# Kernel optimization log

Measured on AMD Instinct MI355X. Metric: run time of the kernel, lower is better.

The kernel has to match this reference:

```python
import jax, jax.numpy as jnp
import numpy as np
from jax import lax

EPS = 1e-5

@jax.custom_vjp
def bin_active(x):
    # forward: sign binarization (original also returns channel-mean of |x|, which is discarded)
    return jnp.sign(x)

def _ba_fwd(x):
    return jnp.sign(x), x

def _ba_bwd(x, g):
    # straight-through estimator: zero grad where |x| >= 1
    return (jnp.where((x >= 1.0) | (x <= -1.0), 0.0, g),)

bin_active.defvjp(_ba_fwd, _ba_bwd)


def setup_inputs() -> dict:
    key = jax.random.key(0)
    k1, k2 = jax.random.split(key)
    N, C_in, H, W_sp = 64, 256, 56, 56
    C_out, K = 256, 3
    x = jax.random.normal(k1, (N, C_in, H, W_sp), dtype=jnp.float32)
    gamma = jnp.ones((C_in,), dtype=jnp.float32)
    beta = jnp.zeros((C_in,), dtype=jnp.float32)
    W = jax.random.normal(k2, (C_out, C_in, K, K), dtype=jnp.float32) * 0.05
    return {"x": x, "gamma": gamma, "beta": beta, "W": W}


def reference(x, gamma, beta, W):
    # BatchNorm2d (training-mode batch stats), affine
    mean = jnp.mean(x, axis=(0, 2, 3), keepdims=True)          # [1,C,1,1]
    var = jnp.var(x, axis=(0, 2, 3), keepdims=True)
    xn = (x - mean) * lax.rsqrt(var + EPS)
    xn = xn * gamma.reshape(1, -1, 1, 1) + beta.reshape(1, -1, 1, 1)
    # binarize activations
    xb = bin_active(xn)
    # Conv2d stride=1 pad=1, no bias, then ReLU
    y = lax.conv_general_dilated(
        xb, W,
        window_strides=(1, 1),
        padding=[(1, 1), (1, 1)],
        dimension_numbers=("NCHW", "OIHW", "NCHW"),
    )
    return jax.nn.relu(y)
```

## Files before the change

kernel.cpp:

```cpp
#include <hip/hip_runtime.h>
#include <hip/hip_bf16.h>
#include <stdint.h>

#define HP 58
#define CIN 256
#define COUT 256
#define HH 56
#define WW 56
#define XROW 14848
#define IMG_STRIDE (HP*XROW)
#define NPIX 200704.0

#define XO    16
#define SROW  928
#define AO    89600
#define LDS_TOTAL 155136

typedef __attribute__((ext_vector_type(4)))  int i32x4;
typedef __attribute__((ext_vector_type(16))) int i32x16;

#define GLDS(g, l) __builtin_amdgcn_global_load_lds( \
    (const __attribute__((address_space(1))) void*)(g), \
    (__attribute__((address_space(3))) void*)(l), 16, 0, 0)

__global__ __launch_bounds__(256) void stats_partial(const float* __restrict__ x,
                                                     double* __restrict__ part) {
  int b = blockIdx.x;
  int c = b >> 6, n = b & 63;
  const float4* p = (const float4*)(x + (size_t)(n*CIN + c) * (HH*WW));
  double s = 0.0, s2 = 0.0;
  for (int i = threadIdx.x; i < 784; i += 256) {
    float4 v = p[i];
    double a0 = v.x, a1 = v.y, a2 = v.z, a3 = v.w;
    s  += (a0 + a1) + (a2 + a3);
    s2 += (a0*a0 + a1*a1) + (a2*a2 + a3*a3);
  }
  for (int off = 32; off > 0; off >>= 1) {
    s  += __shfl_down(s, off);
    s2 += __shfl_down(s2, off);
  }
  __shared__ double red[8];
  int wv = threadIdx.x >> 6, ln = threadIdx.x & 63;
  if (ln == 0) { red[wv*2] = s; red[wv*2+1] = s2; }
  __syncthreads();
  if (threadIdx.x == 0) {
    double ts = ((red[0]+red[2])+red[4])+red[6];
    double t2 = ((red[1]+red[3])+red[5])+red[7];
    part[(size_t)(c*64 + n)*2]     = ts;
    part[(size_t)(c*64 + n)*2 + 1] = t2;
  }
}

__global__ void stats_final(const double* __restrict__ part,
                            const float* __restrict__ gamma,
                            const float* __restrict__ beta,
                            double* __restrict__ prm) {
  int c = threadIdx.x;
  double s = 0.0, s2 = 0.0;
  for (int n = 0; n < 64; ++n) {
    s  += part[(size_t)(c*64+n)*2];
    s2 += part[(size_t)(c*64+n)*2 + 1];
  }
  double mean = s / NPIX;
  double var  = s2 / NPIX - mean*mean;
  double inv  = 1.0 / sqrt(var + 1e-5);
  prm[c*4+0] = mean;
  prm[c*4+1] = (double)gamma[c] * inv;
  prm[c*4+2] = (double)beta[c];
}

__global__ __launch_bounds__(256) void binarize(const float* __restrict__ x,
                                                const double* __restrict__ prm,
                                                int8_t* __restrict__ xb) {
  int b = blockIdx.x;
  int n = b / HP, y = b % HP;
  int8_t* orow = xb + (size_t)(n*HP + y) * XROW;
  if (y == 0 || y == HP-1) {
    int4 z = {0,0,0,0};
    int4* q = (int4*)orow;
    for (int i = threadIdx.x; i < XROW/16; i += 256) q[i] = z;
    return;
  }
  __shared__ char sbuf[WW][260];
  int h  = y - 1;
  int tid = threadIdx.x;
  #pragma unroll
  for (int it = 0; it < 14; ++it) {
    int t = it*256 + tid;
    int c = t / 14, j = t - c*14;
    float4 v = *(const float4*)(x + (size_t)(n*CIN + c)*(HH*WW) + h*WW + j*4);
    double mu = prm[c*4], gi = prm[c*4+1], be = prm[c*4+2];
    #pragma unroll
    for (int e = 0; e < 4; ++e) {
      double xv = (double)((&v.x)[e]);
      double vv = (xv - mu)*gi + be;
      sbuf[j*4+e][c] = vv > 0.0 ? (int8_t)1 : (vv < 0.0 ? (int8_t)-1 : (int8_t)0);
    }
  }
  __syncthreads();
  for (int u = tid; u < 16*58; u += 256) {
    int slot = u / 58, xx = u - slot*58;
    int4 v = {0,0,0,0};
    if (xx >= 1 && xx <= WW) {
      const uint32_t* src = (const uint32_t*)&sbuf[xx-1][slot*16];
      v.x = src[0]; v.y = src[1]; v.z = src[2]; v.w = src[3];
    }
    *(int4*)(orow + u*16) = v;
  }
}

__global__ __launch_bounds__(256) void wrepack(const float* __restrict__ W,
                                               int8_t* __restrict__ Wbr,
                                               float* __restrict__ invs) {
  int co = blockIdx.x, ci = threadIdx.x;
  float w[9]; float mx = 0.f;
  const float* p = W + (size_t)co*(CIN*9) + ci*9;
  #pragma unroll
  for (int t = 0; t < 9; ++t) { w[t] = p[t]; mx = fmaxf(mx, fabsf(w[t])); }
  for (int off = 32; off > 0; off >>= 1) mx = fmaxf(mx, __shfl_xor(mx, off));
  __shared__ float sm[4];
  if ((threadIdx.x & 63) == 0) sm[threadIdx.x >> 6] = mx;
  __syncthreads();
  mx = fmaxf(fmaxf(sm[0], sm[1]), fmaxf(sm[2], sm[3]));
  float s = mx > 0.f ? 127.f / mx : 0.f;
  int off = ((ci >> 6) * 4 + ((ci >> 4) & 3)) * 4096 + co*16 + (ci & 15);
  #pragma unroll
  for (int t = 0; t < 9; ++t) {
    int q = (int)lrintf(w[t] * s);
    q = q > 127 ? 127 : (q < -127 ? -127 : q);
    Wbr[t*65536 + off] = (int8_t)q;
  }
  if (threadIdx.x == 0) invs[co] = mx / 127.f;
}

__global__ __launch_bounds__(512, 2) void conv_gemm(const int8_t* __restrict__ xb,
                                                    const int8_t* __restrict__ Wbr,
                                                    const float* __restrict__ invs,
                                                    float* __restrict__ out) {
  extern __shared__ char smem[];
  int bid = blockIdx.x;
  int swz = (bid & 7) * 112 + (bid >> 3);
  int n_img = swz / 14, rg = swz - n_img * 14;
  int y0 = 1 + rg * 4;

  int tid = threadIdx.x;
  int ln = tid & 63, wid = tid >> 6;
  int wm = wid >> 2, wn = wid & 3;

  size_t xoff = (size_t)n_img * IMG_STRIDE + (size_t)(y0 - 1) * XROW;

  #pragma unroll
  for (int i = 0; i < 11; ++i) {
    int o = tid*16 + i*8192;
    if (o < 6*XROW)
      GLDS(xb + xoff + o, smem + XO + o);
  }

  const int8_t* stSrc = Wbr + tid*16;
  char*         stDst = smem + AO + tid*16;
#define STAGE(SCOFF, BUFQ) do { \
    const int8_t* _s = stSrc + (SCOFF); \
    char* _d = stDst + (BUFQ)*16384; \
    GLDS(_s, _d); GLDS(_s + 8192, _d + 8192); \
  } while (0)

  i32x16 acc[4][2] = {};
  STAGE(0, 0); STAGE(16384, 1); STAGE(32768, 2);

  const char* vA = smem + AO + ((ln >> 5) << 12) + (wm*128 + (ln & 31)) * 16;
  const char* vX = smem + XO + wn*XROW + (ln >> 5)*SROW + ((ln & 31) - 1) * 16;

  i32x4 aA[4][2], bA[2][2], aB[4][2], bB[2][2];

#define LOADF(Q, SU, AV, BV) do { \
    const char* _ab = vA + (Q)*16384; \
    AV[0][0] = *(const i32x4*)(_ab +    0); AV[0][1] = *(const i32x4*)(_ab + 8192); \
    AV[1][0] = *(const i32x4*)(_ab +  512); AV[1][1] = *(const i32x4*)(_ab + 8704); \
    AV[2][0] = *(const i32x4*)(_ab + 1024); AV[2][1] = *(const i32x4*)(_ab + 9216); \
    AV[3][0] = *(const i32x4*)(_ab + 1536); AV[3][1] = *(const i32x4*)(_ab + 9728); \
    const char* _bb = vX + (SU); \
    BV[0][0] = *(const i32x4*)(_bb +    0); BV[0][1] = *(const i32x4*)(_bb + 1856); \
    BV[1][0] = *(const i32x4*)(_bb +  512); BV[1][1] = *(const i32x4*)(_bb + 2368); \
  } while (0)

#define MFMA_ALL(AV, BV) do { \
    __builtin_amdgcn_s_setprio(1); \
    _Pragma("unroll") \
    for (int ks = 0; ks < 2; ++ks) \
      _Pragma("unroll") \
      for (int mt = 0; mt < 4; ++mt) \
        _Pragma("unroll") \
        for (int nt = 0; nt < 2; ++nt) \
          acc[mt][nt] = __builtin_amdgcn_mfma_i32_32x32x32_i8(AV[mt][ks], BV[nt][ks], \
                                                              acc[mt][nt], 0, 0, 0); \
    __builtin_amdgcn_s_setprio(0); \
  } while (0)

#define VMB do { \
    asm volatile("s_waitcnt vmcnt(2)" ::: "memory"); \
    __builtin_amdgcn_s_barrier(); \
  } while (0)

  asm volatile("s_waitcnt vmcnt(4)" ::: "memory");
  __builtin_amdgcn_s_barrier();
  LOADF(0, 0, aA, bA);

  #pragma unroll 1
  for (int t = 0; t < 9; ++t) {
    int kh0 = (t * 11) >> 5,  kw0 = t - kh0*3;
    int t1  = t < 8 ? t + 1 : 8;
    int kh1 = (t1 * 11) >> 5, kw1 = t1 - kh1*3;
    int su0 = kh0*XROW + kw0*16;
    int su1 = su0 + 3712, su2 = su0 + 7424, su3 = su0 + 11136;
    int su4 = kh1*XROW + kw1*16;
    int sA  = 4*t;
    int sc3 = (sA+3 < 36 ? sA+3 : 35) * 16384;
    int sc4 = (sA+4 < 36 ? sA+4 : 35) * 16384;
    int sc5 = (sA+5 < 36 ? sA+5 : 35) * 16384;
    int sc6 = (sA+6 < 36 ? sA+6 : 35) * 16384;

    VMB; STAGE(sc3, 3); LOADF(1, su1, aB, bB); MFMA_ALL(aA, bA);
    VMB; STAGE(sc4, 0); LOADF(2, su2, aA, bA); MFMA_ALL(aB, bB);
    VMB; STAGE(sc5, 1); LOADF(3, su3, aB, bB); MFMA_ALL(aA, bA);
    VMB; STAGE(sc6, 2); LOADF(0, su4, aA, bA); MFMA_ALL(aB, bB);
  }
  asm volatile("s_waitcnt vmcnt(0)" ::: "memory");

  int y_out = y0 + wn - 1;
  size_t ob0 = ((size_t)n_img * COUT) * (HH*WW) + (size_t)y_out * WW;
  #pragma unroll
  for (int mt = 0; mt < 4; ++mt) {
    int cb0 = wm*128 + mt*32 + ((ln >> 5) << 2);
    float4 iv[4];
    #pragma unroll
    for (int q = 0; q < 4; ++q) iv[q] = *(const float4*)(invs + cb0 + 8*q);
    #pragma unroll
    for (int nt = 0; nt < 2; ++nt) {
      int xx = nt*32 + (ln & 31);
      bool ok = (xx >= 1) && (xx <= WW);
      size_t ob = ob0 + (xx - 1);
      #pragma unroll
      for (int r = 0; r < 16; ++r) {
        int q = r >> 2, rr = r & 3;
        int co = cb0 + 8*q + rr;
        float v = fmaxf((float)acc[mt][nt][r] * ((&iv[q].x)[rr]), 0.0f);
        if (ok) out[ob + (size_t)co * (HH*WW)] = v;
      }
    }
  }
}

extern "C" void kernel_launch(void* const* d_in, const int* in_sizes, int n_in,
                              void* d_out, int out_size, void* d_ws, size_t ws_size,
                              hipStream_t stream) {
  const float* x     = (const float*)d_in[0];
  const float* gamma = (const float*)d_in[1];
  const float* beta  = (const float*)d_in[2];
  const float* W     = (const float*)d_in[3];
  float* out = (float*)d_out;

  char* ws = (char*)d_ws;
  double*  part = (double*)ws;
  double*  prm  = (double*)(ws + 262144);
  float*   invs = (float*)(ws + 270336);
  int8_t*  Wbr  = (int8_t*)(ws + 271360);
  int8_t*  xbuf = (int8_t*)(ws + 1048576);

  (void)hipFuncSetAttribute((const void*)conv_gemm,
                            hipFuncAttributeMaxDynamicSharedMemorySize, LDS_TOTAL);

  hipLaunchKernelGGL(wrepack,       dim3(256),    dim3(256), 0, stream, W, Wbr, invs);
  hipLaunchKernelGGL(stats_partial, dim3(256*64), dim3(256), 0, stream, x, part);
  hipLaunchKernelGGL(stats_final,   dim3(1),      dim3(256), 0, stream, part, gamma, beta, prm);
  hipLaunchKernelGGL(binarize,      dim3(64*HP),  dim3(256), 0, stream, x, prm, xbuf);
  hipLaunchKernelGGL(conv_gemm,     dim3(896),    dim3(512), LDS_TOTAL, stream, xbuf, Wbr, invs, out);
}
```

Measured before the change: 276.5 us.

## Make conv GEMM persistent with half-Cout tiles and cross-tile prefetch

Measured after the change: 270.6 us. -2.2%, faster.

```diff
diff --git a/kernel.cpp b/kernel.cpp
--- a/kernel.cpp
+++ b/kernel.cpp
@@ -123,12 +123,14 @@
   __syncthreads();
   mx = fmaxf(fmaxf(sm[0], sm[1]), fmaxf(sm[2], sm[3]));
   float s = mx > 0.f ? 127.f / mx : 0.f;
-  int off = ((ci >> 6) * 4 + ((ci >> 4) & 3)) * 4096 + co*16 + (ci & 15);
+  int h = ci >> 7, q = (ci >> 5) & 3, ks = (ci >> 4) & 1, r = ci & 15;
+  int ch = co >> 7, col = co & 127;
+  int off = h*32768 + ch*16384 + q*4096 + ks*2048 + col*16 + r;
   #pragma unroll
   for (int t = 0; t < 9; ++t) {
-    int q = (int)lrintf(w[t] * s);
-    q = q > 127 ? 127 : (q < -127 ? -127 : q);
-    Wbr[t*65536 + off] = (int8_t)q;
+    int qv = (int)lrintf(w[t] * s);
+    qv = qv > 127 ? 127 : (qv < -127 ? -127 : qv);
+    Wbr[t*65536 + off] = (int8_t)qv;
   }
   if (threadIdx.x == 0) invs[co] = mx / 127.f;
 }
@@ -139,60 +141,54 @@
                                                     float* __restrict__ out) {
   extern __shared__ char smem[];
   int bid = blockIdx.x;
-  int swz = (bid & 7) * 112 + (bid >> 3);
-  int n_img = swz / 14, rg = swz - n_img * 14;
-  int y0 = 1 + rg * 4;
-
   int tid = threadIdx.x;
   int ln = tid & 63, wid = tid >> 6;
-  int wm = wid >> 2, wn = wid & 3;
-
-  size_t xoff = (size_t)n_img * IMG_STRIDE + (size_t)(y0 - 1) * XROW;
-
-  #pragma unroll
-  for (int i = 0; i < 11; ++i) {
-    int o = tid*16 + i*8192;
-    if (o < 6*XROW)
-      GLDS(xb + xoff + o, smem + XO + o);
-  }
-
-  const int8_t* stSrc = Wbr + tid*16;
-  char*         stDst = smem + AO + tid*16;
-#define STAGE(SCOFF, BUFQ) do { \
-    const int8_t* _s = stSrc + (SCOFF); \
-    char* _d = stDst + (BUFQ)*16384; \
+  int wn = wid >> 1, xh = wid & 1;
+
+  const char* vA = smem + AO + ((ln >> 5) << 11) + (ln & 31) * 16;
+  const char* vX = smem + XO + wn*XROW + ((ln >> 5))*SROW + (xh*32 + (ln & 31) - 1) * 16;
+
+  const int8_t* stSrcT = Wbr + tid*16;
+  char*         stDst  = smem + AO + tid*16;
+
+#define STAGE_X(XOFF) do { \
+    _Pragma("unroll") \
+    for (int _i = 0; _i < 11; ++_i) { \
+      int _o = tid*16 + _i*8192; \
+      if (_o < 6*XROW) GLDS(xb + (XOFF) + _o, smem + XO + _o); \
+    } \
+  } while (0)
+
+#define STAGE_A(CHB, S) do { \
+    int _sc = (S) < 18 ? (S) : 17; \
+    const int8_t* _s = stSrcT + (CHB) + _sc*32768;   \
+    char* _d = stDst + ((S) & 3)*16384; \
     GLDS(_s, _d); GLDS(_s + 8192, _d + 8192); \
   } while (0)
 
-  i32x16 acc[4][2] = {};
-  STAGE(0, 0); STAGE(16384, 1); STAGE(32768, 2);
-
-  const char* vA = smem + AO + ((ln >> 5) << 12) + (wm*128 + (ln & 31)) * 16;
-  const char* vX = smem + XO + wn*XROW + (ln >> 5)*SROW + ((ln & 31) - 1) * 16;
-
-  i32x4 aA[4][2], bA[2][2], aB[4][2], bB[2][2];
-
-#define LOADF(Q, SU, AV, BV) do { \
-    const char* _ab = vA + (Q)*16384; \
-    AV[0][0] = *(const i32x4*)(_ab +    0); AV[0][1] = *(const i32x4*)(_ab + 8192); \
-    AV[1][0] = *(const i32x4*)(_ab +  512); AV[1][1] = *(const i32x4*)(_ab + 8704); \
-    AV[2][0] = *(const i32x4*)(_ab + 1024); AV[2][1] = *(const i32x4*)(_ab + 9216); \
-    AV[3][0] = *(const i32x4*)(_ab + 1536); AV[3][1] = *(const i32x4*)(_ab + 9728); \
+  i32x4 aA[4][4], bA[4], aB[4][4], bB[4];
+
+#define LOADF(BUF, SU, AV, BV) do { \
+    const char* _ab = vA + (BUF)*16384; \
+    _Pragma("unroll") \
+    for (int _q = 0; _q < 4; ++_q) { \
+      AV[_q][0] = *(const i32x4*)(_ab + _q*4096 +    0); \
+      AV[_q][1] = *(const i32x4*)(_ab + _q*4096 +  512); \
+      AV[_q][2] = *(const i32x4*)(_ab + _q*4096 + 1024); \
+      AV[_q][3] = *(const i32x4*)(_ab + _q*4096 + 1536); \
+    } \
     const char* _bb = vX + (SU); \
-    BV[0][0] = *(const i32x4*)(_bb +    0); BV[0][1] = *(const i32x4*)(_bb + 1856); \
-    BV[1][0] = *(const i32x4*)(_bb +  512); BV[1][1] = *(const i32x4*)(_bb + 2368); \
+    BV[0] = *(const i32x4*)(_bb +    0); BV[1] = *(const i32x4*)(_bb + 1856); \
+    BV[2] = *(const i32x4*)(_bb + 3712); BV[3] = *(const i32x4*)(_bb + 5568); \
   } while (0)
 
 #define MFMA_ALL(AV, BV) do { \
     __builtin_amdgcn_s_setprio(1); \
     _Pragma("unroll") \
-    for (int ks = 0; ks < 2; ++ks) \
+    for (int _q = 0; _q < 4; ++_q) \
       _Pragma("unroll") \
-      for (int mt = 0; mt < 4; ++mt) \
-        _Pragma("unroll") \
-        for (int nt = 0; nt < 2; ++nt) \
-          acc[mt][nt] = __builtin_amdgcn_mfma_i32_32x32x32_i8(AV[mt][ks], BV[nt][ks], \
-                                                              acc[mt][nt], 0, 0, 0); \
+      for (int _mt = 0; _mt < 4; ++_mt) \
+        acc[_mt] = __builtin_amdgcn_mfma_i32_32x32x32_i8(AV[_q][_mt], BV[_q], acc[_mt], 0, 0, 0); \
     __builtin_amdgcn_s_setprio(0); \
   } while (0)
 
@@ -201,49 +197,75 @@
     __builtin_amdgcn_s_barrier(); \
   } while (0)
 
-  asm volatile("s_waitcnt vmcnt(4)" ::: "memory");
-  __builtin_amdgcn_s_barrier();
-  LOADF(0, 0, aA, bA);
+  const int SUT[9] = { 0*XROW+0*16, 0*XROW+1*16, 0*XROW+2*16,
+                       1*XROW+0*16, 1*XROW+1*16, 1*XROW+2*16,
+                       2*XROW+0*16, 2*XROW+1*16, 2*XROW+2*16 };
+
+  int T0 = bid*7;
+  {
+    int ch = T0 / 896, rem = T0 - ch*896;
+    int img = rem / 14, rg = rem - img*14;
+    size_t xoffp = (size_t)img * IMG_STRIDE + (size_t)(rg*4) * XROW;
+    STAGE_X(xoffp);
+    int chb = ch*16384;
+    STAGE_A(chb, 0); STAGE_A(chb, 1); STAGE_A(chb, 2);
+  }
 
   #pragma unroll 1
-  for (int t = 0; t < 9; ++t) {
-    int kh0 = (t * 11) >> 5,  kw0 = t - kh0*3;
-    int t1  = t < 8 ? t + 1 : 8;
-    int kh1 = (t1 * 11) >> 5, kw1 = t1 - kh1*3;
-    int su0 = kh0*XROW + kw0*16;
-    int su1 = su0 + 3712, su2 = su0 + 7424, su3 = su0 + 11136;
-    int su4 = kh1*XROW + kw1*16;
-    int sA  = 4*t;
-    int sc3 = (sA+3 < 36 ? sA+3 : 35) * 16384;
-    int sc4 = (sA+4 < 36 ? sA+4 : 35) * 16384;
-    int sc5 = (sA+5 < 36 ? sA+5 : 35) * 16384;
-    int sc6 = (sA+6 < 36 ? sA+6 : 35) * 16384;
-
-    VMB; STAGE(sc3, 3); LOADF(1, su1, aB, bB); MFMA_ALL(aA, bA);
-    VMB; STAGE(sc4, 0); LOADF(2, su2, aA, bA); MFMA_ALL(aB, bB);
-    VMB; STAGE(sc5, 1); LOADF(3, su3, aB, bB); MFMA_ALL(aA, bA);
-    VMB; STAGE(sc6, 2); LOADF(0, su4, aA, bA); MFMA_ALL(aB, bB);
-  }
-  asm volatile("s_waitcnt vmcnt(0)" ::: "memory");
-
-  int y_out = y0 + wn - 1;
-  size_t ob0 = ((size_t)n_img * COUT) * (HH*WW) + (size_t)y_out * WW;
-  #pragma unroll
-  for (int mt = 0; mt < 4; ++mt) {
-    int cb0 = wm*128 + mt*32 + ((ln >> 5) << 2);
-    float4 iv[4];
+  for (int i = 0; i < 7; ++i) {
+    int T = bid*7 + i;
+    int ch = T / 896, rem = T - ch*896;
+    int img = rem / 14, rg = rem - img*14;
+    int y0 = 1 + rg*4;
+    int chb = ch*16384;
+
+    i32x16 acc[4] = {};
+
+    asm volatile("s_waitcnt vmcnt(4)" ::: "memory");
+    __builtin_amdgcn_s_barrier();
+    LOADF(0, SUT[0], aA, bA);
+
+    #pragma unroll 1
+    for (int u = 0; u < 9; ++u) {
+      int su0 = SUT[u];
+      int su1 = su0 + 7424;
+      int su2 = (u < 8) ? SUT[u+1] : (SUT[8] + 7424);
+      int s0 = 2*u;
+
+      VMB; STAGE_A(chb, s0+3); LOADF((s0+1)&3, su1, aB, bB); MFMA_ALL(aA, bA);
+      VMB; STAGE_A(chb, s0+4); LOADF((s0+2)&3, su2, aA, bA); MFMA_ALL(aB, bB);
+    }
+
+    asm volatile("s_waitcnt lgkmcnt(0)" ::: "memory");
+    __builtin_amdgcn_s_barrier();
+
+    if (i < 6) {
+      int Tn = T + 1;
+      int chn = Tn / 896, remn = Tn - chn*896;
+      int imgn = remn / 14, rgn = remn - imgn*14;
+      size_t xoffn = (size_t)imgn * IMG_STRIDE + (size_t)(rgn*4) * XROW;
+      STAGE_X(xoffn);
+      int chbn = chn*16384;
+      STAGE_A(chbn, 0); STAGE_A(chbn, 1); STAGE_A(chbn, 2);
+    }
+
+    int cb0 = ch*128 + ((ln >> 5) << 2);
+    int y_out = y0 + wn - 1;
+    size_t ob0 = ((size_t)img * COUT) * (HH*WW) + (size_t)y_out * WW;
+    int xx = xh*32 + (ln & 31);
+    bool ok = (xx >= 1) && (xx <= WW);
+    size_t ob = ob0 + (xx - 1);
     #pragma unroll
-    for (int q = 0; q < 4; ++q) iv[q] = *(const float4*)(invs + cb0 + 8*q);
-    #pragma unroll
-    for (int nt = 0; nt < 2; ++nt) {
-      int xx = nt*32 + (ln & 31);
-      bool ok = (xx >= 1) && (xx <= WW);
-      size_t ob = ob0 + (xx - 1);
+    for (int mt = 0; mt < 4; ++mt) {
+      int cbm = cb0 + mt*32;
+      float4 iv[4];
+      #pragma unroll
+      for (int q = 0; q < 4; ++q) iv[q] = *(const float4*)(invs + cbm + 8*q);
       #pragma unroll
       for (int r = 0; r < 16; ++r) {
         int q = r >> 2, rr = r & 3;
-        int co = cb0 + 8*q + rr;
-        float v = fmaxf((float)acc[mt][nt][r] * ((&iv[q].x)[rr]), 0.0f);
+        int co = cbm + 8*q + rr;
+        float v = fmaxf((float)acc[mt][r] * ((&iv[q].x)[rr]), 0.0f);
         if (ok) out[ob + (size_t)co * (HH*WW)] = v;
       }
     }
@@ -273,5 +295,5 @@
   hipLaunchKernelGGL(stats_partial, dim3(256*64), dim3(256), 0, stream, x, part);
   hipLaunchKernelGGL(stats_final,   dim3(1),      dim3(256), 0, stream, part, gamma, beta, prm);
   hipLaunchKernelGGL(binarize,      dim3(64*HP),  dim3(256), 0, stream, x, prm, xbuf);
-  hipLaunchKernelGGL(conv_gemm,     dim3(896),    dim3(512), LDS_TOTAL, stream, xbuf, Wbr, invs, out);
-}
+  hipLaunchKernelGGL(conv_gemm,     dim3(256),    dim3(512), LDS_TOTAL, stream, xbuf, Wbr, invs, out);
+}
```

## Split output channels across blocks and read activations directly from global

Applied to the files above, without the earlier changes.

Result: slower. 288.5 us (+4.3%).

```diff
diff --git a/kernel.cpp b/kernel.cpp
--- a/kernel.cpp
+++ b/kernel.cpp
@@ -8,13 +8,11 @@
 #define HH 56
 #define WW 56
 #define XROW 14848
+#define SROW 928
 #define IMG_STRIDE (HP*XROW)
 #define NPIX 200704.0
 
-#define XO    16
-#define SROW  928
-#define AO    89600
-#define LDS_TOTAL 155136
+#define LDS_TOTAL 32768
 
 typedef __attribute__((ext_vector_type(4)))  int i32x4;
 typedef __attribute__((ext_vector_type(16))) int i32x16;
@@ -123,114 +121,100 @@
   __syncthreads();
   mx = fmaxf(fmaxf(sm[0], sm[1]), fmaxf(sm[2], sm[3]));
   float s = mx > 0.f ? 127.f / mx : 0.f;
-  int off = ((ci >> 6) * 4 + ((ci >> 4) & 3)) * 4096 + co*16 + (ci & 15);
+  int q = ci >> 6, ks = (ci >> 5) & 1, half = (ci >> 4) & 1, r = ci & 15;
+  int ch = co >> 7, col = co & 127;
+  int off = ch*8192 + (ks*2 + half)*2048 + col*16 + r;
   #pragma unroll
   for (int t = 0; t < 9; ++t) {
-    int q = (int)lrintf(w[t] * s);
-    q = q > 127 ? 127 : (q < -127 ? -127 : q);
-    Wbr[t*65536 + off] = (int8_t)q;
+    int qv = (int)lrintf(w[t] * s);
+    qv = qv > 127 ? 127 : (qv < -127 ? -127 : qv);
+    Wbr[(t*4 + q)*16384 + off] = (int8_t)qv;
   }
   if (threadIdx.x == 0) invs[co] = mx / 127.f;
 }
 
-__global__ __launch_bounds__(512, 2) void conv_gemm(const int8_t* __restrict__ xb,
+__global__ __launch_bounds__(512, 4) void conv_gemm(const int8_t* __restrict__ xb,
                                                     const int8_t* __restrict__ Wbr,
                                                     const float* __restrict__ invs,
                                                     float* __restrict__ out) {
   extern __shared__ char smem[];
   int bid = blockIdx.x;
-  int swz = (bid & 7) * 112 + (bid >> 3);
-  int n_img = swz / 14, rg = swz - n_img * 14;
-  int y0 = 1 + rg * 4;
+  int swz = (bid & 7) * 224 + (bid >> 3);
+  int ch = swz & 1;
+  int g  = swz >> 1;
+  int img = g / 14, rg = g - img*14;
+  int y0 = 1 + rg*4;
 
   int tid = threadIdx.x;
   int ln = tid & 63, wid = tid >> 6;
   int wm = wid >> 2, wn = wid & 3;
 
-  size_t xoff = (size_t)n_img * IMG_STRIDE + (size_t)(y0 - 1) * XROW;
-
-  #pragma unroll
-  for (int i = 0; i < 11; ++i) {
-    int o = tid*16 + i*8192;
-    if (o < 6*XROW)
-      GLDS(xb + xoff + o, smem + XO + o);
-  }
-
-  const int8_t* stSrc = Wbr + tid*16;
-  char*         stDst = smem + AO + tid*16;
-#define STAGE(SCOFF, BUFQ) do { \
-    const int8_t* _s = stSrc + (SCOFF); \
-    char* _d = stDst + (BUFQ)*16384; \
-    GLDS(_s, _d); GLDS(_s + 8192, _d + 8192); \
-  } while (0)
-
-  i32x16 acc[4][2] = {};
-  STAGE(0, 0); STAGE(16384, 1); STAGE(32768, 2);
-
-  const char* vA = smem + AO + ((ln >> 5) << 12) + (wm*128 + (ln & 31)) * 16;
-  const char* vX = smem + XO + wn*XROW + (ln >> 5)*SROW + ((ln & 31) - 1) * 16;
-
-  i32x4 aA[4][2], bA[2][2], aB[4][2], bB[2][2];
-
-#define LOADF(Q, SU, AV, BV) do { \
-    const char* _ab = vA + (Q)*16384; \
-    AV[0][0] = *(const i32x4*)(_ab +    0); AV[0][1] = *(const i32x4*)(_ab + 8192); \
-    AV[1][0] = *(const i32x4*)(_ab +  512); AV[1][1] = *(const i32x4*)(_ab + 8704); \
-    AV[2][0] = *(const i32x4*)(_ab + 1024); AV[2][1] = *(const i32x4*)(_ab + 9216); \
-    AV[3][0] = *(const i32x4*)(_ab + 1536); AV[3][1] = *(const i32x4*)(_ab + 9728); \
-    const char* _bb = vX + (SU); \
-    BV[0][0] = *(const i32x4*)(_bb +    0); BV[0][1] = *(const i32x4*)(_bb + 1856); \
-    BV[1][0] = *(const i32x4*)(_bb +  512); BV[1][1] = *(const i32x4*)(_bb + 2368); \
-  } while (0)
-
-#define MFMA_ALL(AV, BV) do { \
+  const int8_t* xg = xb + (size_t)img*IMG_STRIDE + (size_t)(y0 - 1 + wn)*XROW
+                        + (ln >> 5)*SROW + ((ln & 31) - 1)*16;
+  const char* vA = smem + ((ln >> 5) << 11) + (wm*64 + (ln & 31))*16;
+
+  const int8_t* stSrc = Wbr + ch*8192 + tid*16;
+  char*         stDst = smem + tid*16;
+
+#define STG(S) do { if ((S) < 36) GLDS(stSrc + (S)*16384, stDst + ((S) & 3)*8192); } while (0)
+
+  i32x4 a[2][2], b0[2][2], b1[2][2];
+  i32x16 acc[2][2] = {};
+
+#define BLOAD(SU, BV) do { \
+    BV[0][0] = *(const i32x4*)(xg + (SU)); \
+    BV[0][1] = *(const i32x4*)(xg + (SU) + 1856); \
+    BV[1][0] = *(const i32x4*)(xg + (SU) + 512); \
+    BV[1][1] = *(const i32x4*)(xg + (SU) + 2368); \
+  } while (0)
+
+#define ALOAD(S) do { const char* _ab = vA + ((S) & 3)*8192; \
+    a[0][0] = *(const i32x4*)(_ab);        a[0][1] = *(const i32x4*)(_ab + 4096); \
+    a[1][0] = *(const i32x4*)(_ab + 512);  a[1][1] = *(const i32x4*)(_ab + 4608); \
+  } while (0)
+
+#define MF(BV) do { \
     __builtin_amdgcn_s_setprio(1); \
     _Pragma("unroll") \
-    for (int ks = 0; ks < 2; ++ks) \
+    for (int _ks = 0; _ks < 2; ++_ks) \
       _Pragma("unroll") \
-      for (int mt = 0; mt < 4; ++mt) \
+      for (int _mt = 0; _mt < 2; ++_mt) \
         _Pragma("unroll") \
-        for (int nt = 0; nt < 2; ++nt) \
-          acc[mt][nt] = __builtin_amdgcn_mfma_i32_32x32x32_i8(AV[mt][ks], BV[nt][ks], \
-                                                              acc[mt][nt], 0, 0, 0); \
+        for (int _nt = 0; _nt < 2; ++_nt) \
+          acc[_mt][_nt] = __builtin_amdgcn_mfma_i32_32x32x32_i8(a[_mt][_ks], BV[_nt][_ks], \
+                                                                acc[_mt][_nt], 0, 0, 0); \
     __builtin_amdgcn_s_setprio(0); \
   } while (0)
 
-#define VMB do { \
-    asm volatile("s_waitcnt vmcnt(2)" ::: "memory"); \
+#define VM5 do { \
+    asm volatile("s_waitcnt vmcnt(5)" ::: "memory"); \
     __builtin_amdgcn_s_barrier(); \
   } while (0)
 
-  asm volatile("s_waitcnt vmcnt(4)" ::: "memory");
-  __builtin_amdgcn_s_barrier();
-  LOADF(0, 0, aA, bA);
+  STG(0); STG(1); STG(2);
+  BLOAD(0, b0);
 
   #pragma unroll 1
   for (int t = 0; t < 9; ++t) {
-    int kh0 = (t * 11) >> 5,  kw0 = t - kh0*3;
-    int t1  = t < 8 ? t + 1 : 8;
-    int kh1 = (t1 * 11) >> 5, kw1 = t1 - kh1*3;
-    int su0 = kh0*XROW + kw0*16;
-    int su1 = su0 + 3712, su2 = su0 + 7424, su3 = su0 + 11136;
-    int su4 = kh1*XROW + kw1*16;
-    int sA  = 4*t;
-    int sc3 = (sA+3 < 36 ? sA+3 : 35) * 16384;
-    int sc4 = (sA+4 < 36 ? sA+4 : 35) * 16384;
-    int sc5 = (sA+5 < 36 ? sA+5 : 35) * 16384;
-    int sc6 = (sA+6 < 36 ? sA+6 : 35) * 16384;
-
-    VMB; STAGE(sc3, 3); LOADF(1, su1, aB, bB); MFMA_ALL(aA, bA);
-    VMB; STAGE(sc4, 0); LOADF(2, su2, aA, bA); MFMA_ALL(aB, bB);
-    VMB; STAGE(sc5, 1); LOADF(3, su3, aB, bB); MFMA_ALL(aA, bA);
-    VMB; STAGE(sc6, 2); LOADF(0, su4, aA, bA); MFMA_ALL(aB, bB);
-  }
-  asm volatile("s_waitcnt vmcnt(0)" ::: "memory");
+    int kh = (t*11) >> 5, kw = t - kh*3;
+    int su = kh*XROW + kw*16;
+    int t1 = t < 8 ? t + 1 : 8;
+    int kh1 = (t1*11) >> 5, kw1 = t1 - kh1*3;
+    int sun = kh1*XROW + kw1*16;
+
+    VM5; STG(4*t+3); BLOAD(su +  3712, b1); ALOAD(4*t  ); MF(b0);
+    VM5; STG(4*t+4); BLOAD(su +  7424, b0); ALOAD(4*t+1); MF(b1);
+    VM5; STG(4*t+5); BLOAD(su + 11136, b1); ALOAD(4*t+2); MF(b0);
+    VM5; STG(4*t+6);
+    if (t < 8) BLOAD(sun, b0);
+    ALOAD(4*t+3); MF(b1);
+  }
 
   int y_out = y0 + wn - 1;
-  size_t ob0 = ((size_t)n_img * COUT) * (HH*WW) + (size_t)y_out * WW;
-  #pragma unroll
-  for (int mt = 0; mt < 4; ++mt) {
-    int cb0 = wm*128 + mt*32 + ((ln >> 5) << 2);
+  size_t ob0 = ((size_t)img * COUT)*(HH*WW) + (size_t)y_out*WW;
+  #pragma unroll
+  for (int mt = 0; mt < 2; ++mt) {
+    int cb0 = ch*128 + wm*64 + mt*32 + ((ln >> 5) << 2);
     float4 iv[4];
     #pragma unroll
     for (int q = 0; q < 4; ++q) iv[q] = *(const float4*)(invs + cb0 + 8*q);
@@ -244,7 +228,7 @@
         int q = r >> 2, rr = r & 3;
         int co = cb0 + 8*q + rr;
         float v = fmaxf((float)acc[mt][nt][r] * ((&iv[q].x)[rr]), 0.0f);
-        if (ok) out[ob + (size_t)co * (HH*WW)] = v;
+        if (ok) out[ob + (size_t)co*(HH*WW)] = v;
       }
     }
   }
@@ -273,5 +257,5 @@
   hipLaunchKernelGGL(stats_partial, dim3(256*64), dim3(256), 0, stream, x, part);
   hipLaunchKernelGGL(stats_final,   dim3(1),      dim3(256), 0, stream, part, gamma, beta, prm);
   hipLaunchKernelGGL(binarize,      dim3(64*HP),  dim3(256), 0, stream, x, prm, xbuf);
-  hipLaunchKernelGGL(conv_gemm,     dim3(896),    dim3(512), LDS_TOTAL, stream, xbuf, Wbr, invs, out);
-}
+  hipLaunchKernelGGL(conv_gemm,     dim3(1792),   dim3(512), LDS_TOTAL, stream, xbuf, Wbr, invs, out);
+}
```
